# Kernel optimization log

Hardware: AMD Instinct MI355X
Metric: run time of the kernel (lower is better)

The kernel has to match this reference:

```python
import jax, jax.numpy as jnp
import numpy as np

SEQ, B, E, HID = 512, 32, 256, 256
H2 = 2 * HID              # BiLSTM output / DAG-LSTM hidden size
R, NE, NS, SW = 128, 64, 64, 8
N = NE + NS               # total node slots (entities + relation nodes)
VOCAB, NEL = 50000, 128
CLAMP_C, CLAMP_H = 100.0, 100.0


def _uni(k, shape, fan_in):
    b = 1.0 / np.sqrt(fan_in)
    return jax.random.uniform(k, shape, jnp.float32, -b, b)


def setup_inputs() -> dict:
    key = jax.random.key(0)
    ks = jax.random.split(key, 24)
    inp = {}
    inp["tokens"] = jax.random.randint(ks[0], (SEQ, B), 0, VOCAB)
    inp["entity_spans"] = jax.random.randint(ks[1], (NE, SW), 0, SEQ)
    inp["element_names"] = jax.random.randint(ks[2], (NS, B), 0, NEL)
    inp["H"] = jnp.zeros((N, B, H2), jnp.float32)
    inp["A"] = jnp.zeros((1,), jnp.int32)  # unused by forward (as in original)
    inp["T"] = jnp.broadcast_to(jnp.arange(NS, dtype=jnp.int32)[:, None] + NE, (NS, B))
    inp["S"] = jax.random.randint(ks[3], (NS, B, 2), 0, NE + 32)
    inp["entity_spans_size"] = jnp.full((B,), NE, jnp.int32)
    # learned parameters
    inp["word_emb"] = jax.random.normal(ks[4], (VOCAB, E), jnp.float32)
    inp["elem_emb"] = jax.random.normal(ks[5], (NEL, R), jnp.float32)
    inp["attn_w"] = _uni(ks[6], (1, H2), H2)
    inp["attn_b"] = _uni(ks[7], (1,), H2)
    inp["Wih_f"] = _uni(ks[8], (4 * HID, E), E)
    inp["Whh_f"] = _uni(ks[9], (4 * HID, HID), HID)
    inp["bl_f"] = _uni(ks[10], (4 * HID,), HID)
    inp["Wih_b"] = _uni(ks[11], (4 * HID, E), E)
    inp["Whh_b"] = _uni(ks[12], (4 * HID, HID), HID)
    inp["bl_b"] = _uni(ks[13], (4 * HID,), HID)
    inp["W_ioc"] = _uni(ks[14], (3 * H2, R), R + 2 * H2)
    inp["U_ioc"] = _uni(ks[15], (3 * H2, 2 * H2), R + 2 * H2)
    inp["b_ioc"] = _uni(ks[16], (3 * H2,), R + 2 * H2)
    inp["Wf"] = _uni(ks[17], (H2, R), R + H2)
    inp["Uf"] = _uni(ks[18], (H2, H2), R + H2)
    inp["bf"] = _uni(ks[19], (H2,), R + H2)
    inp["W1"] = _uni(ks[20], (2 * H2, H2), H2)
    inp["b1"] = _uni(ks[21], (2 * H2,), H2)
    inp["W2"] = _uni(ks[22], (2, 2 * H2), 2 * H2)
    inp["b2"] = _uni(ks[23], (2,), 2 * H2)
    return inp


def _lstm_dir(x, Wih, Whh, b, reverse):
    # x: [seq, batch, E]; torch gate order i, f, g, o
    h0 = jnp.zeros((x.shape[1], Whh.shape[1]), x.dtype)

    def step(carry, xt):
        h, c = carry
        g = xt @ Wih.T + h @ Whh.T + b
        i, f, gg, o = jnp.split(g, 4, axis=-1)
        c = jax.nn.sigmoid(f) * c + jax.nn.sigmoid(i) * jnp.tanh(gg)
        h = jax.nn.sigmoid(o) * jnp.tanh(c)
        return (h, c), h

    xs = x[::-1] if reverse else x
    _, hs = jax.lax.scan(step, (h0, h0), xs)
    return hs[::-1] if reverse else hs


def _forward(tokens, entity_spans, element_names, H, T, S, entity_spans_size,
             word_emb, elem_emb, attn_w, attn_b,
             Wih_f, Whh_f, bl_f, Wih_b, Whh_b, bl_b,
             W_ioc, U_ioc, b_ioc, Wf, Uf, bf, W1, b1, W2, b2):
    emb = word_emb[tokens]                                  # [SEQ,B,E]
    fwd = _lstm_dir(emb, Wih_f, Whh_f, bl_f, False)
    bwd = _lstm_dir(emb, Wih_b, Whh_b, bl_b, True)
    blstm = jnp.concatenate([fwd, bwd], axis=-1)            # [SEQ,B,H2]

    # attention pooling over entity spans; original multiplies the softmax
    # weights (which sum to 1) against blstm_out[i], so h_entity = wsum * blstm[i]
    attn = blstm @ attn_w[0] + attn_b[0]                    # [SEQ,B]
    scores = attn[entity_spans]                             # [NE,SW,B]
    wsum = jax.nn.softmax(scores, axis=1).sum(axis=1)       # [NE,B] (== 1 up to fp)
    ne = entity_spans.shape[0]
    H = H.at[:ne].set(wsum[..., None] * blstm[:ne])

    rej = jnp.array([0.999, 0.001], jnp.float32)
    acc0 = jnp.array([0.001, 0.999], jnp.float32)
    n_nodes = H.shape[0]

    def cell(hv, c, e):
        # DAG-LSTM cell: hv [2,H2] input hiddens, c [H2] shared cell state, e [R]
        ioc = e @ W_ioc.T + hv.reshape(-1) @ U_ioc.T + b_ioc
        i, o, ch = jnp.split(ioc, 3)
        f = jax.nn.sigmoid(e @ Wf.T + hv @ Uf.T + bf)       # [2,H2] per-input forget
        c_new = jnp.clip(jnp.sum(f * c[None, :], axis=0)
                         + jax.nn.sigmoid(i) * jnp.tanh(ch), -CLAMP_C, CLAMP_C)
        h = jnp.clip(jax.nn.sigmoid(o) * jnp.tanh(c_new), -CLAMP_H, CLAMP_H)
        return h, c_new

    P0 = jnp.concatenate([jnp.tile(acc0, (ne, 1)),
                          jnp.zeros((n_nodes - ne, 2), jnp.float32)], axis=0)

    def batch_body(c, xs):
        Hb, Sb, Tb, Eb, ent_sz = xs

        def step(carry, inp):
            Hb, Pb, c = carry
            args, tgt, el = inp
            valid = (tgt >= ent_sz) & (el > -1)
            cond = jnp.all(Pb[args, 1] > 0.5) & valid
            h_out, c_new = cell(Hb[args], c, elem_emb[el])
            logits = W2 @ (W1 @ h_out + b1) + b2
            pred = jnp.where(cond, jax.nn.softmax(logits), rej)
            Hb = Hb.at[tgt].set(jnp.where(cond, h_out, Hb[tgt]))
            c = jnp.where(cond, c_new, c)
            Pb = Pb.at[tgt].set(jnp.where(valid, pred, Pb[tgt]))
            return (Hb, Pb, c), None

        (Hb, Pb, c), _ = jax.lax.scan(step, (Hb, P0, c), (Sb, Tb, Eb))
        return c, Pb

    # cell state c rolls sequentially across batches, matching the torch loop order
    xs = (jnp.swapaxes(H, 0, 1), jnp.swapaxes(S, 0, 1), T.T,
          element_names.T, entity_spans_size)
    _, P = jax.lax.scan(batch_body, jnp.zeros((H.shape[-1],), jnp.float32), xs)
    return P.reshape(-1, 2)


def reference(tokens, entity_spans, element_names, H, A, T, S, entity_spans_size,
              word_emb, elem_emb, attn_w, attn_b,
              Wih_f, Whh_f, bl_f, Wih_b, Whh_b, bl_b,
              W_ioc, U_ioc, b_ioc, Wf, Uf, bf, W1, b1, W2, b2):
    return _forward(tokens, entity_spans, element_names, H, T, S, entity_spans_size,
                    word_emb, elem_emb, attn_w, attn_b,
                    Wih_f, Whh_f, bl_f, Wih_b, Whh_b, bl_b,
                    W_ioc, U_ioc, b_ioc, Wf, Uf, bf, W1, b1, W2, b2)
```

## Files before the change

kernel.cpp:

```cpp
#include <hip/hip_runtime.h>
#include <stdint.h>

#define SEQB 512
#define BATCH 32
#define EDIM 256
#define HIDN 256
#define HH2 512
#define RDIM 128
#define NEnt 64
#define NSt 64
#define NNODE 128
#define NHELP 112
#define HPG 14
#define NROWS 3584
#define TERMEVT 0xFFFFFFFFu
#define SCOPE_AGENT __HIP_MEMORY_SCOPE_AGENT

static __device__ __forceinline__ float sigm(float x) { return 1.0f / (1.0f + __expf(-x)); }
static __device__ __forceinline__ float tanh_f(float x) { return 1.0f - 2.0f / (__expf(2.0f * x) + 1.0f); }

static __device__ __forceinline__ void barrier_lds() {
  asm volatile("s_waitcnt lgkmcnt(0)" ::: "memory");
  __builtin_amdgcn_sched_barrier(0);
  __builtin_amdgcn_s_barrier();
}

template<int GATHER, int BIASFIRST>
__global__ __launch_bounds__(256) void gemm_tn(
    const float* __restrict__ A, const int* __restrict__ gidx, const float* __restrict__ gtab,
    const float* __restrict__ B0, const float* __restrict__ B1, int nsplitB,
    const float* __restrict__ bias0, const float* __restrict__ bias1, int nsplitBias,
    float* __restrict__ C, int M, int N, int K)
{
  __shared__ float As[16][132];
  __shared__ float Bs[16][132];
  const int tid = threadIdx.x;
  const int m0 = blockIdx.y * 128, n0 = blockIdx.x * 128;

  const int lrow = tid >> 1;
  const int lk   = (tid & 1) * 8;
  const float* arow;
  if (GATHER) arow = gtab + (size_t)gidx[m0 + lrow] * K + lk;
  else        arow = A + (size_t)(m0 + lrow) * K + lk;
  const int bn = n0 + lrow;
  const float* brow = ((bn < nsplitB) ? (B0 + (size_t)bn * K)
                                      : (B1 + (size_t)(bn - nsplitB) * K)) + lk;

  const int tx = tid & 15, ty = tid >> 4;

  float bb[2][4];
#pragma unroll
  for (int in = 0; in < 2; ++in)
#pragma unroll
    for (int j = 0; j < 4; ++j) bb[in][j] = 0.f;
  if (bias0) {
#pragma unroll
    for (int in = 0; in < 2; ++in)
#pragma unroll
      for (int j = 0; j < 4; ++j) {
        int n = n0 + in * 64 + tx * 4 + j;
        bb[in][j] = (n < nsplitBias) ? bias0[n] : bias1[n - nsplitBias];
      }
  }

  float acc[2][2][4][4];
#pragma unroll
  for (int im = 0; im < 2; ++im)
#pragma unroll
    for (int in = 0; in < 2; ++in)
#pragma unroll
      for (int i = 0; i < 4; ++i)
#pragma unroll
        for (int j = 0; j < 4; ++j)
          acc[im][in][i][j] = BIASFIRST ? bb[in][j] : 0.f;

  float4 pa0 = *(const float4*)(arow);
  float4 pa1 = *(const float4*)(arow + 4);
  float4 pb0 = *(const float4*)(brow);
  float4 pb1 = *(const float4*)(brow + 4);

  int k0 = 0;
  while (true) {
    __syncthreads();
    As[lk + 0][lrow] = pa0.x; As[lk + 1][lrow] = pa0.y;
    As[lk + 2][lrow] = pa0.z; As[lk + 3][lrow] = pa0.w;
    As[lk + 4][lrow] = pa1.x; As[lk + 5][lrow] = pa1.y;
    As[lk + 6][lrow] = pa1.z; As[lk + 7][lrow] = pa1.w;
    Bs[lk + 0][lrow] = pb0.x; Bs[lk + 1][lrow] = pb0.y;
    Bs[lk + 2][lrow] = pb0.z; Bs[lk + 3][lrow] = pb0.w;
    Bs[lk + 4][lrow] = pb1.x; Bs[lk + 5][lrow] = pb1.y;
    Bs[lk + 6][lrow] = pb1.z; Bs[lk + 7][lrow] = pb1.w;
    __syncthreads();

    k0 += 16;
    const bool more = (k0 < K);
    if (more) {
      pa0 = *(const float4*)(arow + k0);
      pa1 = *(const float4*)(arow + k0 + 4);
      pb0 = *(const float4*)(brow + k0);
      pb1 = *(const float4*)(brow + k0 + 4);
    }

#pragma unroll
    for (int k = 0; k < 16; ++k) {
      const float4 av0 = *(const float4*)&As[k][ty * 4];
      const float4 av1 = *(const float4*)&As[k][64 + ty * 4];
      const float4 bv0 = *(const float4*)&Bs[k][tx * 4];
      const float4 bv1 = *(const float4*)&Bs[k][64 + tx * 4];
      const float am[2][4] = {{av0.x, av0.y, av0.z, av0.w},
                              {av1.x, av1.y, av1.z, av1.w}};
      const float bw[2][4] = {{bv0.x, bv0.y, bv0.z, bv0.w},
                              {bv1.x, bv1.y, bv1.z, bv1.w}};
#pragma unroll
      for (int im = 0; im < 2; ++im)
#pragma unroll
        for (int in = 0; in < 2; ++in)
#pragma unroll
          for (int i = 0; i < 4; ++i)
#pragma unroll
            for (int j = 0; j < 4; ++j)
              acc[im][in][i][j] += am[im][i] * bw[in][j];
    }
    if (!more) break;
  }

#pragma unroll
  for (int im = 0; im < 2; ++im)
#pragma unroll
    for (int i = 0; i < 4; ++i) {
      const int m = m0 + im * 64 + ty * 4 + i;
#pragma unroll
      for (int in = 0; in < 2; ++in) {
        float4 o;
        o.x = acc[im][in][i][0] + (BIASFIRST ? 0.f : bb[in][0]);
        o.y = acc[im][in][i][1] + (BIASFIRST ? 0.f : bb[in][1]);
        o.z = acc[im][in][i][2] + (BIASFIRST ? 0.f : bb[in][2]);
        o.w = acc[im][in][i][3] + (BIASFIRST ? 0.f : bb[in][3]);
        *(float4*)&C[(size_t)m * N + n0 + in * 64 + tx * 4] = o;
      }
    }
}

__global__ __launch_bounds__(256, 1) void lstm_esplit(
    const float* __restrict__ Xg,
    const float* __restrict__ Whh_f, const float* __restrict__ Whh_b,
    unsigned long long* __restrict__ hxbuf,
    float* __restrict__ blstm)
{
  const int tid = threadIdx.x;
  const int pid = blockIdx.x;
  const int q = pid >> 6, chain = pid & 63;
  const int d = chain >> 5, b = chain & 31;
  const int j = tid & 63;
  const int g = tid >> 6;
  const int elem = q * 64 + j;
  const int grow = g * 256 + elem;

  const float* W = (d ? Whh_b : Whh_f) + (size_t)grow * 256;
  float4 w4[64];
#pragma unroll
  for (int i = 0; i < 64; ++i) w4[i] = *(const float4*)(W + 4 * i);

  __shared__ float h_lds[HIDN];
  __shared__ float gsL[256];
  float creg = 0.f;
  h_lds[tid] = 0.f;
  __syncthreads();

  const float4* h4 = (const float4*)h_lds;
  const int pe = (tid < q * 64) ? tid : (tid + 64);
  const size_t xgoff = (size_t)d * 1024 + grow;

  for (int it = 0; it < SEQB; ++it) {
    const int t = d ? (SEQB - 1 - it) : it;
    const size_t m = (size_t)t * BATCH + b;
    const float xv = Xg[m * 2048 + xgoff];

    if (tid < 192) {
      const unsigned long long* src =
          &hxbuf[((size_t)(it & 1) * 64 + chain) * 256 + pe];
      unsigned long long qv;
      do { qv = __hip_atomic_load(src, __ATOMIC_RELAXED, SCOPE_AGENT); }
      while ((unsigned)(qv >> 32) != (unsigned)it);
      h_lds[pe] = __uint_as_float((unsigned)qv);
    }
    barrier_lds();

    float a0 = 0.f, a1 = 0.f, a2 = 0.f, a3 = 0.f;
#pragma unroll
    for (int i = 0; i < 64; ++i) {
      const float4 hv = h4[i];
      const float4 wv = w4[i];
      a0 += wv.x * hv.x; a1 += wv.y * hv.y; a2 += wv.z * hv.z; a3 += wv.w * hv.w;
    }
    gsL[tid] = (a0 + a1) + (a2 + a3) + xv;
    barrier_lds();

    if (tid < 64) {
      const float gi = gsL[tid], gf = gsL[64 + tid];
      const float gg = gsL[128 + tid], go = gsL[192 + tid];
      creg = sigm(gf) * creg + sigm(gi) * tanh_f(gg);
      const float hn = sigm(go) * tanh_f(creg);
      h_lds[elem] = hn;
      const unsigned long long pk =
          ((unsigned long long)(unsigned)(it + 1) << 32) |
          (unsigned long long)__float_as_uint(hn);
      __hip_atomic_store(&hxbuf[((size_t)((it + 1) & 1) * 64 + chain) * 256 + elem], pk,
                         __ATOMIC_RELAXED, SCOPE_AGENT);
      blstm[m * HH2 + (size_t)d * HIDN + elem] = hn;
    }
    barrier_lds();
  }
}

__global__ __launch_bounds__(256) void attn_k(const float* __restrict__ blstm,
                                              const float* __restrict__ attn_w,
                                              const float* __restrict__ attn_b,
                                              float* __restrict__ attnv)
{
  const int tid = threadIdx.x;
  const int p = blockIdx.x * 4 + (tid >> 6);
  const int lane = tid & 63;
  const size_t base = (size_t)p * HH2 + lane * 8;
  float4 v0 = *(const float4*)&blstm[base];
  float4 v1 = *(const float4*)&blstm[base + 4];
  float4 w0 = *(const float4*)&attn_w[lane * 8];
  float4 w1 = *(const float4*)&attn_w[lane * 8 + 4];
  float acc = v0.x * w0.x + v0.y * w0.y + v0.z * w0.z + v0.w * w0.w
            + v1.x * w1.x + v1.y * w1.y + v1.z * w1.z + v1.w * w1.w;
#pragma unroll
  for (int off = 32; off > 0; off >>= 1) acc += __shfl_down(acc, off);
  if (lane == 0) attnv[p] = acc + attn_b[0];
}

__global__ __launch_bounds__(64) void entity_prep(const int* __restrict__ spans,
                                                  const float* __restrict__ attnv,
                                                  const float* __restrict__ blstm,
                                                  float* __restrict__ Hent,
                                                  float* __restrict__ P_out)
{
  const int nb = blockIdx.x;
  const int n = nb >> 5, b = nb & 31;
  const int tid = threadIdx.x;
  __shared__ float sc[8];
  if (tid < 8) sc[tid] = attnv[spans[n * 8 + tid] * BATCH + b];
  __syncthreads();
  float mx = sc[0];
#pragma unroll
  for (int w = 1; w < 8; ++w) mx = fmaxf(mx, sc[w]);
  float ex[8]; float ssum = 0.f;
#pragma unroll
  for (int w = 0; w < 8; ++w) { ex[w] = __expf(sc[w] - mx); ssum += ex[w]; }
  float wsum = 0.f;
#pragma unroll
  for (int w = 0; w < 8; ++w) wsum += ex[w] / ssum;
  const size_t base = ((size_t)n * BATCH + b) * HH2;
#pragma unroll
  for (int q = 0; q < 2; ++q) {
    int j = q * 256 + tid * 4;
    float4 v = *(const float4*)&blstm[base + j];
    v.x *= wsum; v.y *= wsum; v.z *= wsum; v.w *= wsum;
    *(float4*)&Hent[base + j] = v;
  }
  if (tid == 0) {
    P_out[((size_t)b * NNODE + n) * 2 + 0] = 0.001f;
    P_out[((size_t)b * NNODE + n) * 2 + 1] = 0.999f;
  }
}

__global__ void pack_ucat(const float* __restrict__ U_ioc, const float* __restrict__ Uf,
                          float* __restrict__ Ucat)
{
  int j = blockIdx.x, tid = threadIdx.x;
  for (int k = tid; k < 512; k += 128) {
    float v;
    if (j < 1536)      v = U_ioc[(size_t)j * 1024 + k];
    else if (j < 3072) v = U_ioc[(size_t)(j - 1536) * 1024 + 512 + k];
    else               v = Uf[(size_t)(j - 3072) * 512 + k];
    Ucat[(size_t)j * 512 + k] = v;
  }
}

__global__ __launch_bounds__(256) void mprep(const float* __restrict__ W1,
                                             const float* __restrict__ b1,
                                             const float* __restrict__ W2,
                                             const float* __restrict__ b2,
                                             float* __restrict__ Mmat,
                                             float* __restrict__ mbv)
{
  const int tid = threadIdx.x;
  for (int j = tid; j < 512; j += 256) {
    float a0 = 0.f, a1 = 0.f;
    for (int m = 0; m < 1024; ++m) {
      float w = W1[(size_t)m * 512 + j];
      a0 += W2[m] * w;
      a1 += W2[1024 + m] * w;
    }
    Mmat[j] = a0; Mmat[512 + j] = a1;
  }
  if (tid < 2) {
    float a = b2[tid];
    for (int m = 0; m < 1024; ++m) a += W2[tid * 1024 + m] * b1[m];
    mbv[tid] = a;
  }
}

__global__ __launch_bounds__(512) void dag_seq(
    const int* __restrict__ S, const int* __restrict__ T, const int* __restrict__ EN,
    const int* __restrict__ entsz,
    const float* __restrict__ WE,
    const float* __restrict__ Mmat, const float* __restrict__ mbv,
    float* __restrict__ Tall, float* __restrict__ hbuf,
    uint32_t* slotbase, uint32_t* arrive,
    const float* __restrict__ Ucat, float* __restrict__ P_out)
{
  const int tid = threadIdx.x;
  __shared__ int   SL[NSt * BATCH * 2];
  __shared__ int   TLt[NSt * BATCH];
  __shared__ int   ELt[NSt * BATCH];
  __shared__ int   eszL[BATCH];
  __shared__ float MmatL[1024];
  __shared__ float mbvL[2];
  __shared__ float pstL[NNODE];
  __shared__ int   evtofL[NSt];
  __shared__ int   confL[NSt];
  __shared__ float red0[2][8], red1[2][8];
  __shared__ uint32_t sslot;

  if (blockIdx.x < NHELP) {
    const int w = blockIdx.x;
    const int row = w * 32 + (tid >> 4);
    const int ks = (tid & 15) * 32;
    float wreg[32];
#pragma unroll
    for (int i = 0; i < 8; ++i) {
      float4 v = *(const float4*)&Ucat[(size_t)row * 512 + ks + i * 4];
      wreg[i * 4 + 0] = v.x; wreg[i * 4 + 1] = v.y; wreg[i * 4 + 2] = v.z; wreg[i * 4 + 3] = v.w;
    }
    uint32_t done = 0;
    const int g = w & 7;
    while (true) {
      if (tid == 0) {
        uint32_t sv;
        while ((sv = __hip_atomic_load(&slotbase[done], __ATOMIC_RELAXED, SCOPE_AGENT)) == 0u) {
          __builtin_amdgcn_s_sleep(1);
        }
        __builtin_amdgcn_fence(__ATOMIC_ACQUIRE, "agent");
        sslot = sv;
      }
      __syncthreads();
      const uint32_t slot = sslot;
      if (slot == TERMEVT) break;
      const float* hv = hbuf + (size_t)done * HH2 + ks;
      float acc = 0.f;
#pragma unroll
      for (int i = 0; i < 8; ++i) {
        float4 v = *(const float4*)&hv[i * 4];
        acc += wreg[i * 4 + 0] * v.x + wreg[i * 4 + 1] * v.y
             + wreg[i * 4 + 2] * v.z + wreg[i * 4 + 3] * v.w;
      }
      acc += __shfl_down(acc, 8);
      acc += __shfl_down(acc, 4);
      acc += __shfl_down(acc, 2);
      acc += __shfl_down(acc, 1);
      if ((tid & 15) == 0) {
        __hip_atomic_store(&Tall[(size_t)slot + row], acc, __ATOMIC_RELAXED, SCOPE_AGENT);
      }
      __syncthreads();
      if (tid == 0) {
        __hip_atomic_fetch_add(&arrive[done * 8 + g], 1u, __ATOMIC_RELEASE, SCOPE_AGENT);
      }
      ++done;
    }
    return;
  }

  for (int i = tid; i < NSt * BATCH * 2; i += 512) SL[i] = S[i];
  for (int i = tid; i < NSt * BATCH; i += 512) { TLt[i] = T[i]; ELt[i] = EN[i]; }
  for (int i = tid; i < 1024; i += 512) MmatL[i] = Mmat[i];
  if (tid < BATCH) eszL[tid] = entsz[tid];
  if (tid < 2) mbvL[tid] = mbv[tid];
  __syncthreads();

  float c = 0.f;
  uint32_t e = 0;
  for (int b = 0; b < BATCH; ++b) {
    barrier_lds();
    const int esz = eszL[b];
    for (int j = tid; j < NNODE; j += 512) pstL[j] = (j < NEnt) ? 0.999f : 0.f;
    if (tid < NSt) { confL[tid] = 0; evtofL[tid] = -1; }
    __syncthreads();
    int fp = 0;

    bool  pfok = false;
    float pt0 = 0.f, pt1 = 0.f, pt2 = 0.f, pt3 = 0.f, pt4 = 0.f, pt5 = 0.f, pt6 = 0.f, pt7 = 0.f;
    float pw0 = 0.f, pw1 = 0.f, pw2 = 0.f, pwf = 0.f;

#define PFETCH(sn)                                                              \
    do {                                                                        \
      pfok = false;                                                             \
      if ((sn) < NSt) {                                                         \
        const int sbn_ = (sn) * BATCH + b;                                      \
        const int na0_ = SL[2 * sbn_], na1_ = SL[2 * sbn_ + 1];                 \
        const int nel_ = ELt[sbn_];                                             \
        if (nel_ >= 0) {                                                        \
          const float* nwe_ = WE + (size_t)nel_ * 2048;                         \
          pw0 = nwe_[tid]; pw1 = nwe_[512 + tid]; pw2 = nwe_[1024 + tid];       \
          pwf = nwe_[1536 + tid];                                               \
        }                                                                       \
        const bool ok0_ = (na0_ < NEnt) || (confL[na0_ - NEnt] != 0);           \
        const bool ok1_ = (na1_ < NEnt) || (confL[na1_ - NEnt] != 0);           \
        if (ok0_ && ok1_) {                                                     \
          const size_t ns0_ = ((size_t)na0_ * BATCH + b) * NROWS;               \
          const size_t ns1_ = ((size_t)na1_ * BATCH + b) * NROWS;               \
          pt0 = Tall[ns0_ + tid];               pt1 = Tall[ns1_ + 1536 + tid];  \
          pt2 = Tall[ns0_ + 512 + tid];         pt3 = Tall[ns1_ + 2048 + tid];  \
          pt4 = Tall[ns0_ + 1024 + tid];        pt5 = Tall[ns1_ + 2560 + tid];  \
          pt6 = Tall[ns0_ + 3072 + tid];        pt7 = Tall[ns1_ + 3072 + tid];  \
          pfok = true;                                                          \
        }                                                                       \
      }                                                                         \
    } while (0)

    PFETCH(0);

    for (int s = 0; s < NSt; ++s) {
      const int sb = s * BATCH + b;
      const int a0 = SL[2 * sb], a1 = SL[2 * sb + 1];
      const int tgt = TLt[sb], el = ELt[sb];
      const bool valid = (tgt >= esz) && (el > -1);
      const float pa0 = pstL[a0], pa1 = pstL[a1];
      const bool cond = valid && (pa0 > 0.5f) && (pa1 > 0.5f);
      if (cond) {
        if (!pfok) {
          const int r0 = (a0 >= NEnt) ? (a0 - NEnt) : -1;
          const int r1 = (a1 >= NEnt) ? (a1 - NEnt) : -1;
          if (tid < 8 && r0 >= 0 && !confL[r0]) {
            const uint32_t ev = (uint32_t)evtofL[r0];
            while (__hip_atomic_load(&arrive[ev * 8 + tid], __ATOMIC_RELAXED, SCOPE_AGENT)
                   < (uint32_t)HPG) { __builtin_amdgcn_s_sleep(1); }
          }
          if (tid >= 8 && tid < 16 && r1 >= 0 && !confL[r1]) {
            const uint32_t ev = (uint32_t)evtofL[r1];
            while (__hip_atomic_load(&arrive[ev * 8 + (tid - 8)], __ATOMIC_RELAXED, SCOPE_AGENT)
                   < (uint32_t)HPG) { __builtin_amdgcn_s_sleep(1); }
          }
          __syncthreads();
          if (tid == 0) {
            __builtin_amdgcn_fence(__ATOMIC_ACQUIRE, "agent");
            int evm = -1;
            if (r0 >= 0 && !confL[r0]) { confL[r0] = 1; if (evtofL[r0] > evm) evm = evtofL[r0]; }
            if (r1 >= 0 && !confL[r1]) { confL[r1] = 1; if (evtofL[r1] > evm) evm = evtofL[r1]; }
            if (evm >= 0) {
              for (int r = 0; r < 32; ++r) {
                const int ev_ = evtofL[r];
                if (ev_ >= 0 && ev_ <= evm) confL[r] = 1;
              }
            }
          }
          __syncthreads();
          const size_t s0 = ((size_t)a0 * BATCH + b) * NROWS;
          const size_t s1 = ((size_t)a1 * BATCH + b) * NROWS;
          pt0 = Tall[s0 + tid];        pt1 = Tall[s1 + 1536 + tid];
          pt2 = Tall[s0 + 512 + tid];  pt3 = Tall[s1 + 2048 + tid];
          pt4 = Tall[s0 + 1024 + tid]; pt5 = Tall[s1 + 2560 + tid];
          pt6 = Tall[s0 + 3072 + tid]; pt7 = Tall[s1 + 3072 + tid];
        }
        const float ii = pw0 + pt0 + pt1;
        const float oo = pw1 + pt2 + pt3;
        const float ch = pw2 + pt4 + pt5;
        const float f0g = sigm(pwf + pt6);
        const float f1g = sigm(pwf + pt7);
        PFETCH(s + 1);
        float cn = (f0g + f1g) * c + sigm(ii) * tanh_f(ch);
        cn = fminf(fmaxf(cn, -100.f), 100.f);
        float hh = sigm(oo) * tanh_f(cn);
        hh = fminf(fmaxf(hh, -100.f), 100.f);
        const bool pubc = (tgt < NEnt + 32);
        if (pubc) {
          __hip_atomic_store(&hbuf[(size_t)e * HH2 + tid], hh, __ATOMIC_RELAXED, SCOPE_AGENT);
        }
        float l0 = MmatL[tid] * hh, l1 = MmatL[512 + tid] * hh;
#pragma unroll
        for (int off = 32; off > 0; off >>= 1) {
          l0 += __shfl_down(l0, off);
          l1 += __shfl_down(l1, off);
        }
        if ((tid & 63) == 0) { red0[fp][tid >> 6] = l0; red1[fp][tid >> 6] = l1; }
        if (pubc) {
          __syncthreads();
          if (tid == 0) {
            evtofL[tgt - NEnt] = (int)e;
            __hip_atomic_store(&slotbase[e],
                               (uint32_t)(((uint32_t)tgt * BATCH + (uint32_t)b) * NROWS),
                               __ATOMIC_RELEASE, SCOPE_AGENT);
          }
        } else {
          barrier_lds();
        }
        float L0 = mbvL[0], L1 = mbvL[1];
#pragma unroll
        for (int wv = 0; wv < 8; ++wv) { L0 += red0[fp][wv]; L1 += red1[fp][wv]; }
        const float mx = fmaxf(L0, L1);
        const float e0 = __expf(L0 - mx), e1 = __expf(L1 - mx);
        const float inv = 1.f / (e0 + e1);
        const float o0 = e0 * inv, o1 = e1 * inv;
        if ((tid & 63) == 0) pstL[tgt] = o1;
        if (tid == 0) {
          P_out[((size_t)b * NNODE + tgt) * 2 + 0] = o0;
          P_out[((size_t)b * NNODE + tgt) * 2 + 1] = o1;
        }
        fp ^= 1;
        c = cn;
        if (pubc) {
          ++e;
          barrier_lds();
        }
      } else {
        PFETCH(s + 1);
        if (tid == 0 && (valid || tgt >= NEnt)) {
          const float o0 = valid ? 0.999f : ((tgt < NEnt) ? 0.001f : 0.f);
          const float o1 = valid ? 0.001f : ((tgt < NEnt) ? 0.999f : 0.f);
          P_out[((size_t)b * NNODE + tgt) * 2 + 0] = o0;
          P_out[((size_t)b * NNODE + tgt) * 2 + 1] = o1;
        }
        if (valid && (tid & 63) == 0) pstL[tgt] = 0.001f;
      }
    }
#undef PFETCH
  }
  if (tid == 0) {
    __hip_atomic_store(&slotbase[e], TERMEVT, __ATOMIC_RELEASE, SCOPE_AGENT);
  }
}

extern "C" void kernel_launch(void* const* d_in, const int* in_sizes, int n_in,
                              void* d_out, int out_size, void* d_ws, size_t ws_size,
                              hipStream_t stream)
{
  const int* tokens = (const int*)d_in[0];
  const int* spans  = (const int*)d_in[1];
  const int* enames = (const int*)d_in[2];
  const int* T      = (const int*)d_in[5];
  const int* S      = (const int*)d_in[6];
  const int* entsz  = (const int*)d_in[7];
  const float* word_emb = (const float*)d_in[8];
  const float* elem_emb = (const float*)d_in[9];
  const float* attn_w = (const float*)d_in[10];
  const float* attn_b = (const float*)d_in[11];
  const float* Wih_f = (const float*)d_in[12];
  const float* Whh_f = (const float*)d_in[13];
  const float* bl_f  = (const float*)d_in[14];
  const float* Wih_b = (const float*)d_in[15];
  const float* Whh_b = (const float*)d_in[16];
  const float* bl_b  = (const float*)d_in[17];
  const float* W_ioc = (const float*)d_in[18];
  const float* U_ioc = (const float*)d_in[19];
  const float* b_ioc = (const float*)d_in[20];
  const float* Wf    = (const float*)d_in[21];
  const float* Uf    = (const float*)d_in[22];
  const float* bf    = (const float*)d_in[23];
  const float* W1    = (const float*)d_in[24];
  const float* b1    = (const float*)d_in[25];
  const float* W2    = (const float*)d_in[26];
  const float* b2    = (const float*)d_in[27];
  float* P_out = (float*)d_out;

  char* ws = (char*)d_ws;
  uint32_t* slotbase = (uint32_t*)(ws + 8192);
  uint32_t* arrive   = (uint32_t*)(ws + 16384);
  float* fws = (float*)(ws + 65536);
  size_t off = 0;
  float* Xg    = fws + off; off += (size_t)16384 * 2048;
  float* blstm = fws + off; off += (size_t)SEQB * BATCH * HH2;
  float* attnv = fws + off; off += (size_t)SEQB * BATCH;
  float* Hent  = fws + off; off += (size_t)2048 * 512;
  float* Tall  = fws + off; off += (size_t)96 * BATCH * NROWS;
  unsigned long long* hxbuf = (unsigned long long*)(fws + off);
  off += (size_t)2 * 64 * 256 * 2;
  float* Ucat  = fws + off; off += (size_t)NROWS * 512;
  float* WE    = fws + off; off += (size_t)128 * 2048;
  float* Mmat  = fws + off; off += 1024;
  float* mbv   = fws + off; off += 16;
  float* hbuf  = fws + off; off += (size_t)1024 * 512;
  const size_t needed = 65536 + off * sizeof(float);
  if (ws_size < needed) return;

  hipMemsetAsync(d_ws, 0, 65536, stream);
  hipMemsetAsync(hxbuf, 0, (size_t)2 * 64 * 256 * 8, stream);

  gemm_tn<1, 0><<<dim3(2048 / 128, 16384 / 128), 256, 0, stream>>>(
      nullptr, tokens, word_emb, Wih_f, Wih_b, 1024, bl_f, bl_b, 1024,
      Xg, 16384, 2048, 256);

  lstm_esplit<<<256, 256, 0, stream>>>(Xg, Whh_f, Whh_b, hxbuf, blstm);

  attn_k<<<4096, 256, 0, stream>>>(blstm, attn_w, attn_b, attnv);
  entity_prep<<<2048, 64, 0, stream>>>(spans, attnv, blstm, Hent, P_out);

  pack_ucat<<<NROWS, 128, 0, stream>>>(U_ioc, Uf, Ucat);
  gemm_tn<0, 1><<<dim3(2048 / 128, 1), 256, 0, stream>>>(
      elem_emb, nullptr, nullptr, W_ioc, Wf, 1536, b_ioc, bf, 1536,
      WE, 128, 2048, 128);
  mprep<<<1, 256, 0, stream>>>(W1, b1, W2, b2, Mmat, mbv);
  gemm_tn<0, 0><<<dim3(NROWS / 128, 2048 / 128), 256, 0, stream>>>(
      Hent, nullptr, nullptr, Ucat, nullptr, 0x40000000, nullptr, nullptr, 0,
      Tall, 2048, NROWS, 512);

  dag_seq<<<NHELP + 1, 512, 0, stream>>>(S, T, enames, entsz, WE, Mmat, mbv,
                                         Tall, hbuf, slotbase, arrive, Ucat, P_out);
}
```

Baseline: 5.497 ms.

## Replace arrival counters with sentinel-filled Tall polling for DAG dependencies

Drops the per-event arrival counters and confirmation bookkeeping between helper blocks and the sequential DAG block. Instead, the relation-node region of Tall is pre-filled with a sentinel pattern, and the consumer polls each loaded value until it differs from the sentinel. This removes barriers and atomic adds from the helpers and the confirmation syncs from the critical path, and it lets prefetch always load speculatively. The trade-offs are an extra memset and correctness that depends on a real result never equalling the sentinel bit pattern. There is also a possible issue with relation slots being reused across batches, since the sentinel is only written once per launch.

```diff
diff --git a/kernel.cpp b/kernel.cpp
--- a/kernel.cpp
+++ b/kernel.cpp
@@ -11,9 +11,9 @@
 #define NSt 64
 #define NNODE 128
 #define NHELP 112
-#define HPG 14
 #define NROWS 3584
 #define TERMEVT 0xFFFFFFFFu
+#define SENTU 0x7F7F7F7Fu
 #define SCOPE_AGENT __HIP_MEMORY_SCOPE_AGENT
 
 static __device__ __forceinline__ float sigm(float x) { return 1.0f / (1.0f + __expf(-x)); }
@@ -311,7 +311,7 @@
     const float* __restrict__ WE,
     const float* __restrict__ Mmat, const float* __restrict__ mbv,
     float* __restrict__ Tall, float* __restrict__ hbuf,
-    uint32_t* slotbase, uint32_t* arrive,
+    uint32_t* slotbase,
     const float* __restrict__ Ucat, float* __restrict__ P_out)
 {
   const int tid = threadIdx.x;
@@ -322,10 +322,8 @@
   __shared__ float MmatL[1024];
   __shared__ float mbvL[2];
   __shared__ float pstL[NNODE];
-  __shared__ int   evtofL[NSt];
-  __shared__ int   confL[NSt];
   __shared__ float red0[2][8], red1[2][8];
-  __shared__ uint32_t sslot;
+  __shared__ uint32_t sslotP[2];
 
   if (blockIdx.x < NHELP) {
     const int w = blockIdx.x;
@@ -338,7 +336,6 @@
       wreg[i * 4 + 0] = v.x; wreg[i * 4 + 1] = v.y; wreg[i * 4 + 2] = v.z; wreg[i * 4 + 3] = v.w;
     }
     uint32_t done = 0;
-    const int g = w & 7;
     while (true) {
       if (tid == 0) {
         uint32_t sv;
@@ -346,10 +343,10 @@
           __builtin_amdgcn_s_sleep(1);
         }
         __builtin_amdgcn_fence(__ATOMIC_ACQUIRE, "agent");
-        sslot = sv;
+        sslotP[done & 1] = sv;
       }
       __syncthreads();
-      const uint32_t slot = sslot;
+      const uint32_t slot = sslotP[done & 1];
       if (slot == TERMEVT) break;
       const float* hv = hbuf + (size_t)done * HH2 + ks;
       float acc = 0.f;
@@ -366,10 +363,6 @@
       if ((tid & 15) == 0) {
         __hip_atomic_store(&Tall[(size_t)slot + row], acc, __ATOMIC_RELAXED, SCOPE_AGENT);
       }
-      __syncthreads();
-      if (tid == 0) {
-        __hip_atomic_fetch_add(&arrive[done * 8 + g], 1u, __ATOMIC_RELEASE, SCOPE_AGENT);
-      }
       ++done;
     }
     return;
@@ -388,17 +381,14 @@
     barrier_lds();
     const int esz = eszL[b];
     for (int j = tid; j < NNODE; j += 512) pstL[j] = (j < NEnt) ? 0.999f : 0.f;
-    if (tid < NSt) { confL[tid] = 0; evtofL[tid] = -1; }
     __syncthreads();
     int fp = 0;
 
-    bool  pfok = false;
     float pt0 = 0.f, pt1 = 0.f, pt2 = 0.f, pt3 = 0.f, pt4 = 0.f, pt5 = 0.f, pt6 = 0.f, pt7 = 0.f;
     float pw0 = 0.f, pw1 = 0.f, pw2 = 0.f, pwf = 0.f;
 
 #define PFETCH(sn)                                                              \
     do {                                                                        \
-      pfok = false;                                                             \
       if ((sn) < NSt) {                                                         \
         const int sbn_ = (sn) * BATCH + b;                                      \
         const int na0_ = SL[2 * sbn_], na1_ = SL[2 * sbn_ + 1];                 \
@@ -408,17 +398,22 @@
           pw0 = nwe_[tid]; pw1 = nwe_[512 + tid]; pw2 = nwe_[1024 + tid];       \
           pwf = nwe_[1536 + tid];                                               \
         }                                                                       \
-        const bool ok0_ = (na0_ < NEnt) || (confL[na0_ - NEnt] != 0);           \
-        const bool ok1_ = (na1_ < NEnt) || (confL[na1_ - NEnt] != 0);           \
-        if (ok0_ && ok1_) {                                                     \
-          const size_t ns0_ = ((size_t)na0_ * BATCH + b) * NROWS;               \
-          const size_t ns1_ = ((size_t)na1_ * BATCH + b) * NROWS;               \
-          pt0 = Tall[ns0_ + tid];               pt1 = Tall[ns1_ + 1536 + tid];  \
-          pt2 = Tall[ns0_ + 512 + tid];         pt3 = Tall[ns1_ + 2048 + tid];  \
-          pt4 = Tall[ns0_ + 1024 + tid];        pt5 = Tall[ns1_ + 2560 + tid];  \
-          pt6 = Tall[ns0_ + 3072 + tid];        pt7 = Tall[ns1_ + 3072 + tid];  \
-          pfok = true;                                                          \
-        }                                                                       \
+        const size_t ns0_ = ((size_t)na0_ * BATCH + b) * NROWS;                 \
+        const size_t ns1_ = ((size_t)na1_ * BATCH + b) * NROWS;                 \
+        pt0 = Tall[ns0_ + tid];               pt1 = Tall[ns1_ + 1536 + tid];    \
+        pt2 = Tall[ns0_ + 512 + tid];         pt3 = Tall[ns1_ + 2048 + tid];    \
+        pt4 = Tall[ns0_ + 1024 + tid];        pt5 = Tall[ns1_ + 2560 + tid];    \
+        pt6 = Tall[ns0_ + 3072 + tid];        pt7 = Tall[ns1_ + 3072 + tid];    \
+      }                                                                         \
+    } while (0)
+
+#define REPOLL(pt, ap)                                                          \
+    do {                                                                        \
+      if (__float_as_uint(pt) == SENTU) {                                       \
+        do {                                                                    \
+          __builtin_amdgcn_s_sleep(2);                                          \
+          pt = __hip_atomic_load((ap), __ATOMIC_RELAXED, SCOPE_AGENT);          \
+        } while (__float_as_uint(pt) == SENTU);                                 \
       }                                                                         \
     } while (0)
 
@@ -432,39 +427,17 @@
       const float pa0 = pstL[a0], pa1 = pstL[a1];
       const bool cond = valid && (pa0 > 0.5f) && (pa1 > 0.5f);
       if (cond) {
-        if (!pfok) {
-          const int r0 = (a0 >= NEnt) ? (a0 - NEnt) : -1;
-          const int r1 = (a1 >= NEnt) ? (a1 - NEnt) : -1;
-          if (tid < 8 && r0 >= 0 && !confL[r0]) {
-            const uint32_t ev = (uint32_t)evtofL[r0];
-            while (__hip_atomic_load(&arrive[ev * 8 + tid], __ATOMIC_RELAXED, SCOPE_AGENT)
-                   < (uint32_t)HPG) { __builtin_amdgcn_s_sleep(1); }
-          }
-          if (tid >= 8 && tid < 16 && r1 >= 0 && !confL[r1]) {
-            const uint32_t ev = (uint32_t)evtofL[r1];
-            while (__hip_atomic_load(&arrive[ev * 8 + (tid - 8)], __ATOMIC_RELAXED, SCOPE_AGENT)
-                   < (uint32_t)HPG) { __builtin_amdgcn_s_sleep(1); }
-          }
-          __syncthreads();
-          if (tid == 0) {
-            __builtin_amdgcn_fence(__ATOMIC_ACQUIRE, "agent");
-            int evm = -1;
-            if (r0 >= 0 && !confL[r0]) { confL[r0] = 1; if (evtofL[r0] > evm) evm = evtofL[r0]; }
-            if (r1 >= 0 && !confL[r1]) { confL[r1] = 1; if (evtofL[r1] > evm) evm = evtofL[r1]; }
-            if (evm >= 0) {
-              for (int r = 0; r < 32; ++r) {
-                const int ev_ = evtofL[r];
-                if (ev_ >= 0 && ev_ <= evm) confL[r] = 1;
-              }
-            }
-          }
-          __syncthreads();
+        {
           const size_t s0 = ((size_t)a0 * BATCH + b) * NROWS;
           const size_t s1 = ((size_t)a1 * BATCH + b) * NROWS;
-          pt0 = Tall[s0 + tid];        pt1 = Tall[s1 + 1536 + tid];
-          pt2 = Tall[s0 + 512 + tid];  pt3 = Tall[s1 + 2048 + tid];
-          pt4 = Tall[s0 + 1024 + tid]; pt5 = Tall[s1 + 2560 + tid];
-          pt6 = Tall[s0 + 3072 + tid]; pt7 = Tall[s1 + 3072 + tid];
+          REPOLL(pt0, &Tall[s0 + tid]);
+          REPOLL(pt2, &Tall[s0 + 512 + tid]);
+          REPOLL(pt4, &Tall[s0 + 1024 + tid]);
+          REPOLL(pt6, &Tall[s0 + 3072 + tid]);
+          REPOLL(pt1, &Tall[s1 + 1536 + tid]);
+          REPOLL(pt3, &Tall[s1 + 2048 + tid]);
+          REPOLL(pt5, &Tall[s1 + 2560 + tid]);
+          REPOLL(pt7, &Tall[s1 + 3072 + tid]);
         }
         const float ii = pw0 + pt0 + pt1;
         const float oo = pw1 + pt2 + pt3;
@@ -490,11 +463,11 @@
         if (pubc) {
           __syncthreads();
           if (tid == 0) {
-            evtofL[tgt - NEnt] = (int)e;
             __hip_atomic_store(&slotbase[e],
                                (uint32_t)(((uint32_t)tgt * BATCH + (uint32_t)b) * NROWS),
                                __ATOMIC_RELEASE, SCOPE_AGENT);
           }
+          ++e;
         } else {
           barrier_lds();
         }
@@ -512,10 +485,6 @@
         }
         fp ^= 1;
         c = cn;
-        if (pubc) {
-          ++e;
-          barrier_lds();
-        }
       } else {
         PFETCH(s + 1);
         if (tid == 0 && (valid || tgt >= NEnt)) {
@@ -528,6 +497,7 @@
       }
     }
 #undef PFETCH
+#undef REPOLL
   }
   if (tid == 0) {
     __hip_atomic_store(&slotbase[e], TERMEVT, __ATOMIC_RELEASE, SCOPE_AGENT);
@@ -568,7 +538,6 @@
 
   char* ws = (char*)d_ws;
   uint32_t* slotbase = (uint32_t*)(ws + 8192);
-  uint32_t* arrive   = (uint32_t*)(ws + 16384);
   float* fws = (float*)(ws + 65536);
   size_t off = 0;
   float* Xg    = fws + off; off += (size_t)16384 * 2048;
@@ -588,6 +557,8 @@
 
   hipMemsetAsync(d_ws, 0, 65536, stream);
   hipMemsetAsync(hxbuf, 0, (size_t)2 * 64 * 256 * 8, stream);
+  hipMemsetAsync(Tall + (size_t)NEnt * BATCH * NROWS, 0x7F,
+                 (size_t)32 * BATCH * NROWS * sizeof(float), stream);
 
   gemm_tn<1, 0><<<dim3(2048 / 128, 16384 / 128), 256, 0, stream>>>(
       nullptr, tokens, word_emb, Wih_f, Wih_b, 1024, bl_f, bl_b, 1024,
@@ -608,5 +579,5 @@
       Tall, 2048, NROWS, 512);
 
   dag_seq<<<NHELP + 1, 512, 0, stream>>>(S, T, enames, entsz, WE, Mmat, mbv,
-                                         Tall, hbuf, slotbase, arrive, Ucat, P_out);
-}
+                                         Tall, hbuf, slotbase, Ucat, P_out);
+}
```

Result: faster. 5.157 ms (-6.2%).
